# Performance work log

Hardware: AMD Instinct MI355X
Metric: run time of the kernel (lower is better)

The kernel has to match this reference:

```python
import jax, jax.numpy as jnp
import numpy as np

EPS = 1e-5
GROUPS = 32
HEADS = 8
RES_SCALE = 0.7071067811865476  # 1/sqrt(2)


def group_norm(x, groups, weight=None, bias=None):
    # x: [b, c, t]; normalize over (c//groups, t) per group, like torch GroupNorm
    b, c, t = x.shape
    xg = x.reshape(b, groups, (c // groups) * t)
    mean = xg.mean(axis=-1, keepdims=True)
    var = xg.var(axis=-1, keepdims=True)
    xg = (xg - mean) * jax.lax.rsqrt(var + EPS)
    x = xg.reshape(b, c, t)
    if weight is not None:
        x = x * weight[None, :, None] + bias[None, :, None]
    return x


def setup_inputs() -> dict:
    key = jax.random.key(0)
    ks = jax.random.split(key, 7)
    b, c, hh, ww = 8, 512, 32, 32
    return {
        "x": jax.random.normal(ks[0], (b, c, hh, ww), dtype=jnp.float32),
        "gn_w": jax.random.uniform(ks[1], (c,), dtype=jnp.float32, minval=0.5, maxval=1.5),
        "gn_b": jax.random.normal(ks[2], (c,), dtype=jnp.float32) * 0.1,
        "qkv_w": jax.random.normal(ks[3], (3 * c, c), dtype=jnp.float32) * (c ** -0.5),
        "qkv_b": jax.random.normal(ks[4], (3 * c,), dtype=jnp.float32) * 0.02,
        "proj_w": jax.random.normal(ks[5], (c, c), dtype=jnp.float32) * 0.02,
        "proj_b": jax.random.normal(ks[6], (c,), dtype=jnp.float32) * 0.02,
    }


def reference(x, gn_w, gn_b, qkv_w, qkv_b, proj_w, proj_b):
    b, c, hh, ww = x.shape
    t = hh * ww
    ch = c // HEADS
    xf = x.reshape(b, c, t)
    xn = group_norm(xf, GROUPS, gn_w, gn_b)
    # 1x1 conv -> GEMM: [b, 3c, t]
    qkv = jnp.einsum('oc,bct->bot', qkv_w, xn) + qkv_b[None, :, None]
    # split order: per head contiguous [q_ch; k_ch; v_ch]
    qkv = qkv.reshape(b * HEADS, 3 * ch, t)
    q, k, v = jnp.split(qkv, 3, axis=1)
    scale = ch ** -0.25
    w = jnp.einsum('bct,bcs->bts', q * scale, k * scale)
    w = jax.nn.softmax(w.astype(jnp.float32), axis=-1).astype(qkv.dtype)
    a = jnp.einsum('bts,bcs->bct', w, v).reshape(b, c, t)
    h = jnp.einsum('oc,bct->bot', proj_w, a) + proj_b[None, :, None]
    out = group_norm(RES_SCALE * xn + h, GROUPS)  # functional group_norm: no affine
    return out.reshape(b, c, hh, ww)
```

## Files before the change

kernel.cpp:

```cpp
#include <hip/hip_runtime.h>


typedef unsigned short u16;
typedef __attribute__((ext_vector_type(8))) short short8v;
typedef __attribute__((ext_vector_type(4))) float float4v;

constexpr int NB = 8, NC = 512, NT = 1024, CPG = 16;
#define EPSV 1e-5f
#define RES_SCALE 0.7071067811865476f
#define QK_SCALE 0.35355339059327376f
#define LOG2E 1.4426950408889634f

static __device__ __forceinline__ u16 f2bf(float f) {
  unsigned int u = __builtin_bit_cast(unsigned int, f);
  u = (u + 0x7fffu + ((u >> 16) & 1u)) >> 16;
  return (u16)u;
}
static __device__ __forceinline__ float exp2_fast(float x) {
  float r;
  asm("v_exp_f32 %0, %1" : "=v"(r) : "v"(x));
  return r;
}

template<bool AFFINE>
__global__ __launch_bounds__(256) void groupnorm_kernel(
    const float* __restrict__ src0, const float* __restrict__ gw,
    const float* __restrict__ gb, float* __restrict__ dst0)
{
  const int tid = threadIdx.x;
  const int b = blockIdx.x >> 5;
  const int g = blockIdx.x & 31;
  const size_t off = ((size_t)(b * NC + g * CPG)) * NT;
  const float* src = src0 + off;
  float* dst = dst0 + off;

  const float4* s4 = (const float4*)src;
  float sum = 0.f, sq = 0.f;
  #pragma unroll 4
  for (int i = tid; i < CPG * NT / 4; i += 256) {
    float4 v = s4[i];
    sum += v.x + v.y + v.z + v.w;
    sq  += v.x * v.x + v.y * v.y + v.z * v.z + v.w * v.w;
  }
  #pragma unroll
  for (int off2 = 32; off2; off2 >>= 1) {
    sum += __shfl_xor(sum, off2);
    sq  += __shfl_xor(sq,  off2);
  }
  __shared__ float rs[4], rq[4], stats[2];
  const int wave = tid >> 6, lane = tid & 63;
  if (lane == 0) { rs[wave] = sum; rq[wave] = sq; }
  __syncthreads();
  if (tid == 0) {
    float S = rs[0] + rs[1] + rs[2] + rs[3];
    float Q = rq[0] + rq[1] + rq[2] + rq[3];
    float mean = S * (1.0f / (CPG * NT));
    float var  = Q * (1.0f / (CPG * NT)) - mean * mean;
    stats[0] = mean;
    stats[1] = rsqrtf(var + EPSV);
  }
  __syncthreads();
  const float mean = stats[0], rstd = stats[1];
  float4* d4 = (float4*)dst;
  #pragma unroll 4
  for (int i = tid; i < CPG * NT / 4; i += 256) {
    float a, c2;
    if (AFFINE) {
      int ch = g * CPG + (i >> 8);
      float wv = gw[ch];
      a  = rstd * wv;
      c2 = gb[ch] - mean * a;
    } else {
      a  = rstd;
      c2 = -mean * rstd;
    }
    float4 v = s4[i];
    v.x = v.x * a + c2; v.y = v.y * a + c2;
    v.z = v.z * a + c2; v.w = v.w * a + c2;
    d4[i] = v;
  }
}

__global__ __launch_bounds__(256) void convert_w_kernel(
    const float* __restrict__ qw, const float* __restrict__ pw,
    u16* __restrict__ qwb, u16* __restrict__ pwb)
{
  const int i = blockIdx.x * 256 + threadIdx.x;
  const float* in;
  u16* out;
  int j;
  if (i < 98304) { in = qw; out = qwb; j = i; }
  else           { in = pw; out = pwb; j = i - 98304; }
  const float4 a = *(const float4*)(in + (size_t)j * 8);
  const float4 b = *(const float4*)(in + (size_t)j * 8 + 4);
  short8v o;
  o[0] = (short)f2bf(a.x); o[1] = (short)f2bf(a.y);
  o[2] = (short)f2bf(a.z); o[3] = (short)f2bf(a.w);
  o[4] = (short)f2bf(b.x); o[5] = (short)f2bf(b.y);
  o[6] = (short)f2bf(b.z); o[7] = (short)f2bf(b.w);
  *(short8v*)(out + (size_t)j * 8) = o;
}

__global__ __launch_bounds__(256) void transpose_kernel(
    const float* __restrict__ xnf, u16* __restrict__ xbt)
{
  __shared__ __attribute__((aligned(16))) u16 T[64 * 80];
  const int tid = threadIdx.x;
  const int tt = blockIdx.x, cc = blockIdx.y, b = blockIdx.z;
  const int c = tid >> 2, tch = (tid & 3) * 16;
  const float* src = xnf + ((size_t)b * NC + cc * 64 + c) * NT + tt * 64 + tch;
  #pragma unroll
  for (int j = 0; j < 4; j++) {
    float4 v = *(const float4*)(src + j * 4);
    T[(tch + j * 4 + 0) * 80 + c] = f2bf(v.x);
    T[(tch + j * 4 + 1) * 80 + c] = f2bf(v.y);
    T[(tch + j * 4 + 2) * 80 + c] = f2bf(v.z);
    T[(tch + j * 4 + 3) * 80 + c] = f2bf(v.w);
  }
  __syncthreads();
  const int t = tid >> 2, cp = (tid & 3) * 2;
  u16* dst = xbt + ((size_t)b * NT + tt * 64 + t) * NC + cc * 64;
  #pragma unroll
  for (int q = 0; q < 2; q++)
    *(short8v*)(dst + (cp + q) * 8) = *(const short8v*)(T + t * 80 + (cp + q) * 8);
}

template<int MODE>
__global__ __launch_bounds__(256) void mfma_gemm_kernel(
    const u16* __restrict__ Wb, const float* __restrict__ bias,
    const u16* __restrict__ Bt, u16* __restrict__ qkT,
    u16* __restrict__ vN, float* __restrict__ outF,
    const float* __restrict__ xnf)
{
  __shared__ __attribute__((aligned(16))) u16 lds[(MODE == 1) ? 17408 : 16384];
  u16* As = lds;
  u16* Bs = lds + 8192;
  const int tid = threadIdx.x;
  const int w = tid >> 6, l = tid & 63, lr = l & 15, lg = l >> 4;
  const int wm = (w >> 1) * 64, wn = (w & 1) * 64;
  const int bn = blockIdx.x * 128, bm = blockIdx.y * 128, b = blockIdx.z;

  const u16* Ag = Wb + (size_t)bm * 512;
  const u16* Bg = Bt + ((size_t)b * NT + bn) * 512;
  const int sr = tid >> 3;
  const int sc = tid & 7;

  float4v acc[4][4];
  #pragma unroll
  for (int i = 0; i < 4; i++)
    #pragma unroll
    for (int j = 0; j < 4; j++) acc[i][j] = (float4v){0.f, 0.f, 0.f, 0.f};

  for (int k0 = 0; k0 < 512; k0 += 64) {
    short8v av[4], bv[4];
    #pragma unroll
    for (int j = 0; j < 4; j++) {
      const int m = sr + 32 * j;
      av[j] = *(const short8v*)(Ag + (size_t)m * 512 + k0 + sc * 8);
      bv[j] = *(const short8v*)(Bg + (size_t)m * 512 + k0 + sc * 8);
    }
    __syncthreads();
    #pragma unroll
    for (int j = 0; j < 4; j++) {
      const int m = sr + 32 * j;
      *(short8v*)(As + m * 64 + ((sc ^ (m & 7)) * 8)) = av[j];
      *(short8v*)(Bs + m * 64 + ((sc ^ (m & 7)) * 8)) = bv[j];
    }
    __syncthreads();
    #pragma unroll
    for (int kk = 0; kk < 2; kk++) {
      short8v af[4], bf[4];
      #pragma unroll
      for (int mi = 0; mi < 4; mi++) {
        const int m = wm + mi * 16 + lr;
        af[mi] = *(const short8v*)(As + m * 64 + (((kk * 4 + lg) ^ (m & 7)) * 8));
      }
      #pragma unroll
      for (int ni = 0; ni < 4; ni++) {
        const int n = wn + ni * 16 + lr;
        bf[ni] = *(const short8v*)(Bs + n * 64 + (((kk * 4 + lg) ^ (n & 7)) * 8));
      }
      #pragma unroll
      for (int mi = 0; mi < 4; mi++)
        #pragma unroll
        for (int ni = 0; ni < 4; ni++)
          acc[mi][ni] = __builtin_amdgcn_mfma_f32_16x16x32_bf16(af[mi], bf[ni], acc[mi][ni], 0, 0, 0);
    }
  }

  if (MODE == 0) {
    #pragma unroll
    for (int mi = 0; mi < 4; mi++) {
      const int m0 = bm + wm + mi * 16 + lg * 4;
      const int head = m0 / 192;
      const int r0 = m0 - head * 192;
      const float4 bv4 = *(const float4*)(bias + m0);
      if (r0 < 128) {
        const float scl = (r0 < 64) ? QK_SCALE * LOG2E : QK_SCALE;
        const int col = head * 128 + r0;
        #pragma unroll
        for (int ni = 0; ni < 4; ni++) {
          const int t = bn + wn + ni * 16 + lr;
          unsigned int lo = (unsigned)f2bf((acc[mi][ni][0] + bv4.x) * scl) |
                            ((unsigned)f2bf((acc[mi][ni][1] + bv4.y) * scl) << 16);
          unsigned int hi = (unsigned)f2bf((acc[mi][ni][2] + bv4.z) * scl) |
                            ((unsigned)f2bf((acc[mi][ni][3] + bv4.w) * scl) << 16);
          *(uint2*)(qkT + ((size_t)b * NT + t) * 1024 + col) = make_uint2(lo, hi);
        }
      } else {
        const int vc = head * 64 + (r0 - 128);
        #pragma unroll
        for (int ni = 0; ni < 4; ni++) {
          const int t = bn + wn + ni * 16 + lr;
          vN[((size_t)b * NC + vc + 0) * NT + t] = f2bf(acc[mi][ni][0] + bv4.x);
          vN[((size_t)b * NC + vc + 1) * NT + t] = f2bf(acc[mi][ni][1] + bv4.y);
          vN[((size_t)b * NC + vc + 2) * NT + t] = f2bf(acc[mi][ni][2] + bv4.z);
          vN[((size_t)b * NC + vc + 3) * NT + t] = f2bf(acc[mi][ni][3] + bv4.w);
        }
      }
    }
  } else {
    float* Cs = (float*)lds;
    for (int ph = 0; ph < 2; ph++) {
      __syncthreads();
      if ((w >> 1) == ph) {
        #pragma unroll
        for (int mi = 0; mi < 4; mi++)
          #pragma unroll
          for (int ni = 0; ni < 4; ni++) {
            const int rr = mi * 16 + lg * 4;
            const int cc2 = wn + ni * 16 + lr;
            #pragma unroll
            for (int r = 0; r < 4; r++)
              Cs[(rr + r) * 136 + cc2] = acc[mi][ni][r];
          }
      }
      __syncthreads();
      const int mloc = tid >> 2;
      const int m = bm + ph * 64 + mloc;
      const float bv = bias[m];
      const int cb = (tid & 3) * 32;
      const float* cr = Cs + mloc * 136 + cb;
      const float* xr = xnf + ((size_t)b * NC + m) * NT + bn + cb;
      float* yr = outF + ((size_t)b * NC + m) * NT + bn + cb;
      #pragma unroll
      for (int j = 0; j < 8; j++) {
        float4 c4 = *(const float4*)(cr + j * 4);
        float4 x4 = *(const float4*)(xr + j * 4);
        float4 o;
        o.x = c4.x + bv + RES_SCALE * x4.x;
        o.y = c4.y + bv + RES_SCALE * x4.y;
        o.z = c4.z + bv + RES_SCALE * x4.z;
        o.w = c4.w + bv + RES_SCALE * x4.w;
        *(float4*)(yr + j * 4) = o;
      }
    }
  }
}

__global__ __launch_bounds__(256, 4) void attn_mfma_kernel(
    const u16* __restrict__ qkT, const u16* __restrict__ vN, u16* __restrict__ aT)
{
  __shared__ __attribute__((aligned(16))) u16 lds[5 * 4096];
  u16* K0 = lds;
  u16* K1 = lds + 4096;
  u16* V0 = lds + 8192;
  u16* V1 = lds + 12288;
  u16* Ps = lds + 16384;
  const int tid = threadIdx.x;
  const int w = tid >> 6, l = tid & 63, lr = l & 15, lg = l >> 4;
  const int bh = blockIdx.y;
  const int b = bh >> 3, h = bh & 7;
  const int t0 = blockIdx.x * 64;

  const u16* qbase = qkT + (size_t)b * NT * 1024 + h * 128;
  const u16* kbase = qbase + 64;
  const u16* vbase = vN + ((size_t)b * NC + h * 64) * NT;

  const size_t qrow = (size_t)(t0 + w * 16 + lr) * 1024;
  const short8v qa0 = *(const short8v*)(qbase + qrow + lg * 8);
  const short8v qa1 = *(const short8v*)(qbase + qrow + 32 + lg * 8);

  const int srow_st = tid >> 3;
  const int scl = tid & 7;

  float4v out[4];
  #pragma unroll
  for (int nc = 0; nc < 4; nc++) out[nc] = (float4v){0.f, 0.f, 0.f, 0.f};
  float ps[4] = {0.f, 0.f, 0.f, 0.f};

  short8v kr[2], vr[2];
  #pragma unroll
  for (int j = 0; j < 2; j++) {
    const int row = srow_st + 32 * j;
    kr[j] = *(const short8v*)(kbase + (size_t)row * 1024 + scl * 8);
    vr[j] = *(const short8v*)(vbase + (size_t)row * NT + scl * 8);
  }
  #pragma unroll
  for (int j = 0; j < 2; j++) {
    const int row = srow_st + 32 * j;
    *(short8v*)(K0 + row * 64 + ((scl ^ (row & 7)) * 8)) = kr[j];
    *(short8v*)(V0 + row * 64 + ((scl ^ (row & 7)) * 8)) = vr[j];
  }
  __syncthreads();

  for (int it = 0; it < 16; ++it) {
    const u16* Kc = (it & 1) ? K1 : K0;
    const u16* Vc = (it & 1) ? V1 : V0;
    if (it < 15) {
      const int s0n = (it + 1) * 64;
      #pragma unroll
      for (int j = 0; j < 2; j++) {
        const int row = srow_st + 32 * j;
        kr[j] = *(const short8v*)(kbase + (size_t)(s0n + row) * 1024 + scl * 8);
        vr[j] = *(const short8v*)(vbase + (size_t)row * NT + s0n + scl * 8);
      }
    }

    float4v sacc[4];
    #pragma unroll
    for (int n = 0; n < 4; n++) sacc[n] = (float4v){0.f, 0.f, 0.f, 0.f};
    #pragma unroll
    for (int n = 0; n < 4; n++) {
      const int srow = n * 16 + lr;
      short8v kb0 = *(const short8v*)(Kc + srow * 64 + ((lg ^ (srow & 7)) * 8));
      short8v kb1 = *(const short8v*)(Kc + srow * 64 + (((4 + lg) ^ (srow & 7)) * 8));
      sacc[n] = __builtin_amdgcn_mfma_f32_16x16x32_bf16(qa0, kb0, sacc[n], 0, 0, 0);
      sacc[n] = __builtin_amdgcn_mfma_f32_16x16x32_bf16(qa1, kb1, sacc[n], 0, 0, 0);
    }

    #pragma unroll
    for (int n = 0; n < 4; n++) {
      #pragma unroll
      for (int r = 0; r < 4; r++) {
        float p = exp2_fast(sacc[n][r]);
        ps[r] += p;
        const int t = w * 16 + lg * 4 + r;
        Ps[t * 64 + ((n * 16 + lr) ^ ((t & 7) << 3))] =
            (u16)(__builtin_bit_cast(unsigned int, p) >> 16);
      }
    }

    #pragma unroll
    for (int kc = 0; kc < 2; kc++) {
      const int prow = w * 16 + lr;
      short8v pa = *(const short8v*)(Ps + prow * 64 + ((kc * 32 + lg * 8) ^ ((prow & 7) << 3)));
      #pragma unroll
      for (int nc = 0; nc < 4; nc++) {
        const int crow = nc * 16 + lr;
        short8v vb = *(const short8v*)(Vc + crow * 64 + (((kc * 4 + lg) ^ (crow & 7)) * 8));
        out[nc] = __builtin_amdgcn_mfma_f32_16x16x32_bf16(pa, vb, out[nc], 0, 0, 0);
      }
    }

    if (it < 15) {
      u16* Kn = (it & 1) ? K0 : K1;
      u16* Vn = (it & 1) ? V0 : V1;
      #pragma unroll
      for (int j = 0; j < 2; j++) {
        const int row = srow_st + 32 * j;
        *(short8v*)(Kn + row * 64 + ((scl ^ (row & 7)) * 8)) = kr[j];
        *(short8v*)(Vn + row * 64 + ((scl ^ (row & 7)) * 8)) = vr[j];
      }
      __syncthreads();
    }
  }

  #pragma unroll
  for (int r = 0; r < 4; r++) {
    ps[r] += __shfl_xor(ps[r], 1);
    ps[r] += __shfl_xor(ps[r], 2);
    ps[r] += __shfl_xor(ps[r], 4);
    ps[r] += __shfl_xor(ps[r], 8);
  }

  __syncthreads();
  u16* At = lds;
  float inv[4];
  #pragma unroll
  for (int r = 0; r < 4; r++) inv[r] = 1.0f / ps[r];
  #pragma unroll
  for (int nc = 0; nc < 4; nc++)
    #pragma unroll
    for (int r = 0; r < 4; r++)
      At[(w * 16 + lg * 4 + r) * 80 + nc * 16 + lr] = f2bf(out[nc][r] * inv[r]);
  __syncthreads();
  const int t = tid >> 2, cp = (tid & 3) * 2;
  u16* dst = aT + ((size_t)b * NT + t0 + t) * NC + h * 64;
  #pragma unroll
  for (int q = 0; q < 2; q++)
    *(short8v*)(dst + (cp + q) * 8) = *(const short8v*)(At + t * 80 + (cp + q) * 8);
}

extern "C" void kernel_launch(void* const* d_in, const int* in_sizes, int n_in,
                              void* d_out, int out_size, void* d_ws, size_t ws_size,
                              hipStream_t stream)
{
  const float* x      = (const float*)d_in[0];
  const float* gn_w   = (const float*)d_in[1];
  const float* gn_b   = (const float*)d_in[2];
  const float* qkv_w  = (const float*)d_in[3];
  const float* qkv_b  = (const float*)d_in[4];
  const float* proj_w = (const float*)d_in[5];
  const float* proj_b = (const float*)d_in[6];
  float* out = (float*)d_out;

  float* xn  = (float*)d_ws;
  u16* base16 = (u16*)(xn + (size_t)NB * NC * NT);
  u16* xbt = base16;
  u16* qkT = xbt + (size_t)NB * NT * NC;
  u16* vN  = qkT + (size_t)NB * NT * 1024;
  u16* aT  = vN + (size_t)NB * NC * NT;
  u16* qwb = aT + (size_t)NB * NT * NC;
  u16* pwb = qwb + 1536 * 512;

  groupnorm_kernel<true><<<dim3(NB * 32), 256, 0, stream>>>(x, gn_w, gn_b, xn);
  convert_w_kernel<<<dim3(512), 256, 0, stream>>>(qkv_w, proj_w, qwb, pwb);
  transpose_kernel<<<dim3(16, 8, NB), 256, 0, stream>>>(xn, xbt);
  mfma_gemm_kernel<0><<<dim3(8, 12, NB), 256, 0, stream>>>(qwb, qkv_b, xbt, qkT, vN, nullptr, nullptr);
  attn_mfma_kernel<<<dim3(16, 64), 256, 0, stream>>>(qkT, vN, aT);
  mfma_gemm_kernel<1><<<dim3(8, 4, NB), 256, 0, stream>>>(pwb, proj_b, aT, nullptr, nullptr, out, xn);
  groupnorm_kernel<false><<<dim3(NB * 32), 256, 0, stream>>>(out, nullptr, nullptr, out);
}
```

Baseline: 184.2 us.

## Use direct global-to-LDS loads in GEMM and attention, merge prep kernels

Replaces the register-staged global->LDS copies in both the MFMA GEMM and the attention kernel with global_load_lds async loads into double-buffered LDS. The GEMM k-step also drops from 64 to 32 with a new XOR swizzle. The attention kernel remaps its grid to a 1D launch with a head-interleaved block order and raises wave priority around the MFMA sections. The weight conversion and transpose kernels are fused into one launch. Together these aim to cut register pressure, LDS store instructions, barriers and launch overhead, at the cost of more waitcnt/barrier steps per k-tile and a tighter swizzle layout that must match the direct-load lane mapping.

```diff
diff --git a/kernel.cpp b/kernel.cpp
--- a/kernel.cpp
+++ b/kernel.cpp
@@ -81,32 +81,30 @@
   }
 }
 
-__global__ __launch_bounds__(256) void convert_w_kernel(
+__global__ __launch_bounds__(256) void prep_kernel(
+    const float* __restrict__ xnf, u16* __restrict__ xbt,
     const float* __restrict__ qw, const float* __restrict__ pw,
     u16* __restrict__ qwb, u16* __restrict__ pwb)
 {
-  const int i = blockIdx.x * 256 + threadIdx.x;
-  const float* in;
-  u16* out;
-  int j;
-  if (i < 98304) { in = qw; out = qwb; j = i; }
-  else           { in = pw; out = pwb; j = i - 98304; }
-  const float4 a = *(const float4*)(in + (size_t)j * 8);
-  const float4 b = *(const float4*)(in + (size_t)j * 8 + 4);
-  short8v o;
-  o[0] = (short)f2bf(a.x); o[1] = (short)f2bf(a.y);
-  o[2] = (short)f2bf(a.z); o[3] = (short)f2bf(a.w);
-  o[4] = (short)f2bf(b.x); o[5] = (short)f2bf(b.y);
-  o[6] = (short)f2bf(b.z); o[7] = (short)f2bf(b.w);
-  *(short8v*)(out + (size_t)j * 8) = o;
-}
-
-__global__ __launch_bounds__(256) void transpose_kernel(
-    const float* __restrict__ xnf, u16* __restrict__ xbt)
-{
   __shared__ __attribute__((aligned(16))) u16 T[64 * 80];
+  const int x = blockIdx.x;
   const int tid = threadIdx.x;
-  const int tt = blockIdx.x, cc = blockIdx.y, b = blockIdx.z;
+  if (x >= 1024) {
+    const int i = (x - 1024) * 256 + tid;
+    const float* in; u16* out; int j;
+    if (i < 98304) { in = qw; out = qwb; j = i; }
+    else           { in = pw; out = pwb; j = i - 98304; }
+    const float4 a = *(const float4*)(in + (size_t)j * 8);
+    const float4 b = *(const float4*)(in + (size_t)j * 8 + 4);
+    short8v o;
+    o[0] = (short)f2bf(a.x); o[1] = (short)f2bf(a.y);
+    o[2] = (short)f2bf(a.z); o[3] = (short)f2bf(a.w);
+    o[4] = (short)f2bf(b.x); o[5] = (short)f2bf(b.y);
+    o[6] = (short)f2bf(b.z); o[7] = (short)f2bf(b.w);
+    *(short8v*)(out + (size_t)j * 8) = o;
+    return;
+  }
+  const int tt = x & 15, cc = (x >> 4) & 7, b = x >> 7;
   const int c = tid >> 2, tch = (tid & 3) * 16;
   const float* src = xnf + ((size_t)b * NC + cc * 64 + c) * NT + tt * 64 + tch;
   #pragma unroll
@@ -133,8 +131,6 @@
     const float* __restrict__ xnf)
 {
   __shared__ __attribute__((aligned(16))) u16 lds[(MODE == 1) ? 17408 : 16384];
-  u16* As = lds;
-  u16* Bs = lds + 8192;
   const int tid = threadIdx.x;
   const int w = tid >> 6, l = tid & 63, lr = l & 15, lg = l >> 4;
   const int wm = (w >> 1) * 64, wn = (w & 1) * 64;
@@ -142,8 +138,13 @@
 
   const u16* Ag = Wb + (size_t)bm * 512;
   const u16* Bg = Bt + ((size_t)b * NT + bn) * 512;
-  const int sr = tid >> 3;
-  const int sc = tid & 7;
+
+  const int srow = w * 16 + (l >> 2);
+  const int scg  = (l & 3) ^ ((l >> 3) & 3);
+  const u16* ap0 = Ag + (size_t)srow * 512 + scg * 8;
+  const u16* bp0 = Bg + (size_t)srow * 512 + scg * 8;
+  char* ldsb = (char*)lds;
+  char* adst0 = ldsb + w * 1024;
 
   float4v acc[4][4];
   #pragma unroll
@@ -151,40 +152,46 @@
     #pragma unroll
     for (int j = 0; j < 4; j++) acc[i][j] = (float4v){0.f, 0.f, 0.f, 0.f};
 
-  for (int k0 = 0; k0 < 512; k0 += 64) {
-    short8v av[4], bv[4];
-    #pragma unroll
-    for (int j = 0; j < 4; j++) {
-      const int m = sr + 32 * j;
-      av[j] = *(const short8v*)(Ag + (size_t)m * 512 + k0 + sc * 8);
-      bv[j] = *(const short8v*)(Bg + (size_t)m * 512 + k0 + sc * 8);
-    }
-    __syncthreads();
-    #pragma unroll
-    for (int j = 0; j < 4; j++) {
-      const int m = sr + 32 * j;
-      *(short8v*)(As + m * 64 + ((sc ^ (m & 7)) * 8)) = av[j];
-      *(short8v*)(Bs + m * 64 + ((sc ^ (m & 7)) * 8)) = bv[j];
-    }
-    __syncthreads();
-    #pragma unroll
-    for (int kk = 0; kk < 2; kk++) {
-      short8v af[4], bf[4];
-      #pragma unroll
-      for (int mi = 0; mi < 4; mi++) {
-        const int m = wm + mi * 16 + lr;
-        af[mi] = *(const short8v*)(As + m * 64 + (((kk * 4 + lg) ^ (m & 7)) * 8));
-      }
-      #pragma unroll
-      for (int ni = 0; ni < 4; ni++) {
-        const int n = wn + ni * 16 + lr;
-        bf[ni] = *(const short8v*)(Bs + n * 64 + (((kk * 4 + lg) ^ (n & 7)) * 8));
-      }
-      #pragma unroll
-      for (int mi = 0; mi < 4; mi++)
-        #pragma unroll
-        for (int ni = 0; ni < 4; ni++)
-          acc[mi][ni] = __builtin_amdgcn_mfma_f32_16x16x32_bf16(af[mi], bf[ni], acc[mi][ni], 0, 0, 0);
+  #pragma unroll
+  for (int r = 0; r < 2; r++) {
+    __builtin_amdgcn_global_load_lds(ap0 + r * 64 * 512, adst0 + r * 4096, 16, 0, 0);
+    __builtin_amdgcn_global_load_lds(bp0 + r * 64 * 512, adst0 + 8192 + r * 4096, 16, 0, 0);
+  }
+  asm volatile("s_waitcnt vmcnt(0)" ::: "memory");
+  __builtin_amdgcn_s_barrier();
+
+  for (int ks = 0; ks < 16; ++ks) {
+    const int buf = ks & 1;
+    if (ks < 15) {
+      const size_t k0n = (size_t)(ks + 1) * 32;
+      char* an = ldsb + (buf ^ 1) * 16384 + w * 1024;
+      #pragma unroll
+      for (int r = 0; r < 2; r++) {
+        __builtin_amdgcn_global_load_lds(ap0 + k0n + r * 64 * 512, an + r * 4096, 16, 0, 0);
+        __builtin_amdgcn_global_load_lds(bp0 + k0n + r * 64 * 512, an + 8192 + r * 4096, 16, 0, 0);
+      }
+    }
+    const u16* au = lds + buf * 8192;
+    const u16* bu = au + 4096;
+    short8v af[4], bf[4];
+    #pragma unroll
+    for (int mi = 0; mi < 4; mi++) {
+      const int m = wm + mi * 16 + lr;
+      af[mi] = *(const short8v*)(au + m * 32 + ((lg ^ ((m >> 1) & 3)) * 8));
+    }
+    #pragma unroll
+    for (int ni = 0; ni < 4; ni++) {
+      const int n = wn + ni * 16 + lr;
+      bf[ni] = *(const short8v*)(bu + n * 32 + ((lg ^ ((n >> 1) & 3)) * 8));
+    }
+    #pragma unroll
+    for (int mi = 0; mi < 4; mi++)
+      #pragma unroll
+      for (int ni = 0; ni < 4; ni++)
+        acc[mi][ni] = __builtin_amdgcn_mfma_f32_16x16x32_bf16(af[mi], bf[ni], acc[mi][ni], 0, 0, 0);
+    if (ks < 15) {
+      asm volatile("s_waitcnt vmcnt(0)" ::: "memory");
+      __builtin_amdgcn_s_barrier();
     }
   }
 
@@ -262,16 +269,12 @@
     const u16* __restrict__ qkT, const u16* __restrict__ vN, u16* __restrict__ aT)
 {
   __shared__ __attribute__((aligned(16))) u16 lds[5 * 4096];
-  u16* K0 = lds;
-  u16* K1 = lds + 4096;
-  u16* V0 = lds + 8192;
-  u16* V1 = lds + 12288;
-  u16* Ps = lds + 16384;
   const int tid = threadIdx.x;
   const int w = tid >> 6, l = tid & 63, lr = l & 15, lg = l >> 4;
-  const int bh = blockIdx.y;
+  const int L = blockIdx.x;
+  const int bh = (L & 7) * 8 + ((L >> 3) & 7);
+  const int t0 = (L >> 6) * 64;
   const int b = bh >> 3, h = bh & 7;
-  const int t0 = blockIdx.x * 64;
 
   const u16* qbase = qkT + (size_t)b * NT * 1024 + h * 128;
   const u16* kbase = qbase + 64;
@@ -281,45 +284,47 @@
   const short8v qa0 = *(const short8v*)(qbase + qrow + lg * 8);
   const short8v qa1 = *(const short8v*)(qbase + qrow + 32 + lg * 8);
 
-  const int srow_st = tid >> 3;
-  const int scl = tid & 7;
+  const int strow = w * 8 + (l >> 3);
+  const int scg = (l & 7) ^ (l >> 3);
+  const u16* kp0 = kbase + (size_t)strow * 1024 + scg * 8;
+  const u16* vp0 = vbase + (size_t)strow * 1024 + scg * 8;
+  char* ldsb = (char*)lds;
+  u16* Ps = lds + 16384;
 
   float4v out[4];
   #pragma unroll
   for (int nc = 0; nc < 4; nc++) out[nc] = (float4v){0.f, 0.f, 0.f, 0.f};
   float ps[4] = {0.f, 0.f, 0.f, 0.f};
 
-  short8v kr[2], vr[2];
-  #pragma unroll
-  for (int j = 0; j < 2; j++) {
-    const int row = srow_st + 32 * j;
-    kr[j] = *(const short8v*)(kbase + (size_t)row * 1024 + scl * 8);
-    vr[j] = *(const short8v*)(vbase + (size_t)row * NT + scl * 8);
-  }
-  #pragma unroll
-  for (int j = 0; j < 2; j++) {
-    const int row = srow_st + 32 * j;
-    *(short8v*)(K0 + row * 64 + ((scl ^ (row & 7)) * 8)) = kr[j];
-    *(short8v*)(V0 + row * 64 + ((scl ^ (row & 7)) * 8)) = vr[j];
-  }
-  __syncthreads();
+  #pragma unroll
+  for (int r = 0; r < 2; r++) {
+    __builtin_amdgcn_global_load_lds(kp0 + (size_t)r * 32 * 1024,
+                                     ldsb + w * 1024 + r * 4096, 16, 0, 0);
+    __builtin_amdgcn_global_load_lds(vp0 + (size_t)r * 32 * 1024,
+                                     ldsb + 16384 + w * 1024 + r * 4096, 16, 0, 0);
+  }
+  asm volatile("s_waitcnt vmcnt(0)" ::: "memory");
+  __builtin_amdgcn_s_barrier();
 
   for (int it = 0; it < 16; ++it) {
-    const u16* Kc = (it & 1) ? K1 : K0;
-    const u16* Vc = (it & 1) ? V1 : V0;
+    const int buf = it & 1;
     if (it < 15) {
-      const int s0n = (it + 1) * 64;
-      #pragma unroll
-      for (int j = 0; j < 2; j++) {
-        const int row = srow_st + 32 * j;
-        kr[j] = *(const short8v*)(kbase + (size_t)(s0n + row) * 1024 + scl * 8);
-        vr[j] = *(const short8v*)(vbase + (size_t)row * NT + s0n + scl * 8);
-      }
-    }
+      const size_t s0n = (size_t)(it + 1) * 64;
+      char* kd = ldsb + (buf ^ 1) * 8192 + w * 1024;
+      char* vd = ldsb + 16384 + (buf ^ 1) * 8192 + w * 1024;
+      #pragma unroll
+      for (int r = 0; r < 2; r++) {
+        __builtin_amdgcn_global_load_lds(kp0 + (s0n + r * 32) * 1024, kd + r * 4096, 16, 0, 0);
+        __builtin_amdgcn_global_load_lds(vp0 + s0n + (size_t)r * 32 * 1024, vd + r * 4096, 16, 0, 0);
+      }
+    }
+    const u16* Kc = lds + buf * 4096;
+    const u16* Vc = lds + 8192 + buf * 4096;
 
     float4v sacc[4];
     #pragma unroll
     for (int n = 0; n < 4; n++) sacc[n] = (float4v){0.f, 0.f, 0.f, 0.f};
+    __builtin_amdgcn_s_setprio(1);
     #pragma unroll
     for (int n = 0; n < 4; n++) {
       const int srow = n * 16 + lr;
@@ -328,6 +333,7 @@
       sacc[n] = __builtin_amdgcn_mfma_f32_16x16x32_bf16(qa0, kb0, sacc[n], 0, 0, 0);
       sacc[n] = __builtin_amdgcn_mfma_f32_16x16x32_bf16(qa1, kb1, sacc[n], 0, 0, 0);
     }
+    __builtin_amdgcn_s_setprio(0);
 
     #pragma unroll
     for (int n = 0; n < 4; n++) {
@@ -341,6 +347,7 @@
       }
     }
 
+    __builtin_amdgcn_s_setprio(1);
     #pragma unroll
     for (int kc = 0; kc < 2; kc++) {
       const int prow = w * 16 + lr;
@@ -352,17 +359,11 @@
         out[nc] = __builtin_amdgcn_mfma_f32_16x16x32_bf16(pa, vb, out[nc], 0, 0, 0);
       }
     }
+    __builtin_amdgcn_s_setprio(0);
 
     if (it < 15) {
-      u16* Kn = (it & 1) ? K0 : K1;
-      u16* Vn = (it & 1) ? V0 : V1;
-      #pragma unroll
-      for (int j = 0; j < 2; j++) {
-        const int row = srow_st + 32 * j;
-        *(short8v*)(Kn + row * 64 + ((scl ^ (row & 7)) * 8)) = kr[j];
-        *(short8v*)(Vn + row * 64 + ((scl ^ (row & 7)) * 8)) = vr[j];
-      }
-      __syncthreads();
+      asm volatile("s_waitcnt vmcnt(0)" ::: "memory");
+      __builtin_amdgcn_s_barrier();
     }
   }
 
@@ -415,10 +416,9 @@
   u16* pwb = qwb + 1536 * 512;
 
   groupnorm_kernel<true><<<dim3(NB * 32), 256, 0, stream>>>(x, gn_w, gn_b, xn);
-  convert_w_kernel<<<dim3(512), 256, 0, stream>>>(qkv_w, proj_w, qwb, pwb);
-  transpose_kernel<<<dim3(16, 8, NB), 256, 0, stream>>>(xn, xbt);
+  prep_kernel<<<dim3(1536), 256, 0, stream>>>(xn, xbt, qkv_w, proj_w, qwb, pwb);
   mfma_gemm_kernel<0><<<dim3(8, 12, NB), 256, 0, stream>>>(qwb, qkv_b, xbt, qkT, vN, nullptr, nullptr);
-  attn_mfma_kernel<<<dim3(16, 64), 256, 0, stream>>>(qkT, vN, aT);
+  attn_mfma_kernel<<<dim3(1024), 256, 0, stream>>>(qkT, vN, aT);
   mfma_gemm_kernel<1><<<dim3(8, 4, NB), 256, 0, stream>>>(pwb, proj_b, aT, nullptr, nullptr, out, xn);
-  groupnorm_kernel<false><<<dim3(NB * 32), 256, 0, stream>>>(out, nullptr, nullptr, out);
-}
+  groupnorm_kernel<false><<<dim3(256), 256, 0, stream>>>(out, nullptr, nullptr, out);
+}
```

After: 167.2 us. 9.2% less time.
